# Kernel optimization log

Hardware: AMD Instinct MI355X
Metric: run time of the kernel (lower is better)

## Reference

```python
import jax, jax.numpy as jnp
import numpy as np

B, T, C, H = 2, 2048, 1024, 16
D = C // H
CURV = 1.0  # clamp_curvature(1.0) -> 1.0
EPS = 1e-5


def layer_norm(x, w, b):
    mu = jnp.mean(x, axis=-1, keepdims=True)
    var = jnp.var(x, axis=-1, keepdims=True)
    return (x - mu) * jax.lax.rsqrt(var + EPS) * w + b


def mobius_addition(x, y, c):
    xn2 = jnp.sum(x * x, axis=-1, keepdims=True)
    yn2 = jnp.sum(y * y, axis=-1, keepdims=True)
    ip = jnp.sum(x * y, axis=-1, keepdims=True)
    num = (1 + 2 * c * ip + c * yn2) * x + (1 - c * xn2) * y
    den = 1 + 2 * c * ip + (c ** 2) * xn2 * yn2
    return num / den


def scaling_factor(x, c):
    xn2 = jnp.sum(x * x, axis=-1, keepdims=True)
    return 2.0 / (1.0 + c * xn2)


def expmap(x, v, c):
    lam = scaling_factor(x, c)
    vn = jnp.linalg.norm(v, axis=-1, keepdims=True)
    second = (1.0 / c ** 0.5) * jnp.tanh(jnp.sqrt(c * lam * vn ** 2 / 2.0)) * v / vn
    return mobius_addition(x, second, c)


def logmap(x, u, c):
    lam = scaling_factor(x, c)
    m = mobius_addition(-x, u, c)
    mn = jnp.linalg.norm(m, axis=-1, keepdims=True)
    cf = 2.0 / (lam * c ** 0.5)
    arg = jnp.clip(jnp.sqrt(c * mn), -0.999, 0.999)
    return cf * jnp.arctanh(arg) * m / mn


def calc_reference_point(x):
    # shift-right by one token, zero at position 0
    return jnp.pad(x[:, :-1, :], ((0, 0), (1, 0), (0, 0)))


def causal_attention(q, k, v):
    # q,k,v: [B,H,T,D]
    scores = jnp.einsum('bhqd,bhkd->bhqk', q, k) / np.sqrt(D).astype(np.float32)
    mask = jnp.tril(jnp.ones((T, T), dtype=bool))
    scores = jnp.where(mask, scores, -jnp.inf)
    att = jax.nn.softmax(scores, axis=-1)
    return jnp.einsum('bhqk,bhkd->bhqd', att, v)


def setup_inputs() -> dict:
    key = jax.random.key(0)
    ks = jax.random.split(key, 6)
    s = 0.02
    return {
        'x': jax.random.normal(ks[0], (B, T, C), jnp.float32),
        'ln1_w': jnp.ones((C,), jnp.float32),
        'ln1_b': jnp.zeros((C,), jnp.float32),
        'W_attn': jax.random.normal(ks[1], (C, 3 * C), jnp.float32) * s,
        'b_attn': jnp.zeros((3 * C,), jnp.float32),
        'W_aproj': jax.random.normal(ks[2], (C, C), jnp.float32) * s,
        'b_aproj': jnp.zeros((C,), jnp.float32),
        'ln2_w': jnp.ones((C,), jnp.float32),
        'ln2_b': jnp.zeros((C,), jnp.float32),
        'W_fc': jax.random.normal(ks[3], (C, 4 * C), jnp.float32) * s,
        'b_fc': jnp.zeros((4 * C,), jnp.float32),
        'W_mproj': jax.random.normal(ks[4], (4 * C, C), jnp.float32) * s,
        'b_mproj': jnp.zeros((C,), jnp.float32),
    }


def reference(x, ln1_w, ln1_b, W_attn, b_attn, W_aproj, b_aproj,
              ln2_w, ln2_b, W_fc, b_fc, W_mproj, b_mproj):
    c = CURV
    # --- attention branch ---
    xn = layer_norm(x, ln1_w, ln1_b)
    ref = calc_reference_point(xn)
    xt = logmap(ref, xn, c)
    qkv = xt @ W_attn + b_attn
    q, k, v = jnp.split(qkv, 3, axis=-1)
    q = q.reshape(B, T, H, D).transpose(0, 2, 1, 3)
    k = k.reshape(B, T, H, D).transpose(0, 2, 1, 3)
    v = v.reshape(B, T, H, D).transpose(0, 2, 1, 3)
    y = causal_attention(q, k, v)
    y = y.transpose(0, 2, 1, 3).reshape(B, T, C)
    y = expmap(ref, y, c)  # map_back_after_attention=True
    y = y @ W_aproj + b_aproj
    x = x + y
    # --- MLP branch (no expmap since map_back_after_attention) ---
    h = layer_norm(x, ln2_w, ln2_b)
    h = jax.nn.gelu(h @ W_fc + b_fc, approximate=False)
    h = h @ W_mproj + b_mproj
    return x + h
```

## Files before the change

kernel.cpp:

```cpp
#include <hip/hip_runtime.h>
#include <hip/hip_bf16.h>
#include <math.h>

#define BDIM 2
#define TSEQ 2048
#define CDIM 1024
#define HNUM 16
#define NROW (BDIM*TSEQ)
#define AST 88

typedef __attribute__((ext_vector_type(8))) short bf16x8_t;
typedef __attribute__((ext_vector_type(4))) float f32x4_t;

__device__ inline float bf2f(__hip_bfloat16 h) { return __bfloat162float(h); }

__device__ inline void unpack8(uint4 u, float* f) {
  unsigned v[4] = {u.x, u.y, u.z, u.w};
  #pragma unroll
  for (int i = 0; i < 4; ++i) {
    union { unsigned u2; float f2; } a, b;
    a.u2 = v[i] << 16;
    b.u2 = v[i] & 0xffff0000u;
    f[2*i]   = a.f2;
    f[2*i+1] = b.f2;
  }
}

__device__ inline void gload16(const void* g, void* l) {
  __builtin_amdgcn_global_load_lds(
      (const __attribute__((address_space(1))) void*)g,
      (__attribute__((address_space(3))) void*)l, 16, 0, 0);
}

template<int N> __device__ inline void waitcnt_vm() {
  asm volatile("s_waitcnt vmcnt(%0)" :: "i"(N) : "memory");
}

__global__ __launch_bounds__(256) void zero32_kernel(float* p, int n) {
  int i = blockIdx.x * 256 + threadIdx.x;
  if (i < n) p[i] = 0.f;
}

__global__ __launch_bounds__(256) void convT_kernel(const float* __restrict__ src,
    __hip_bfloat16* __restrict__ dst, int K, int N)
{
  __shared__ float tile[32][33];
  const int k0 = blockIdx.x * 32, n0 = blockIdx.y * 32;
  const int tr  = threadIdx.x >> 3;
  const int tc4 = (threadIdx.x & 7) * 4;
  float4 v = *(const float4*)(src + (size_t)(k0 + tr) * N + n0 + tc4);
  tile[tr][tc4+0] = v.x; tile[tr][tc4+1] = v.y;
  tile[tr][tc4+2] = v.z; tile[tr][tc4+3] = v.w;
  __syncthreads();
  union { ushort4 u; __hip_bfloat16 h[4]; } o;
  #pragma unroll
  for (int j = 0; j < 4; ++j) o.h[j] = __float2bfloat16(tile[tc4+j][tr]);
  *(ushort4*)(dst + (size_t)(n0 + tr) * K + k0 + tc4) = o.u;
}

__device__ inline void blk_reduce3(float& a, float& b, float& c, float* red) {
  const int lane = threadIdx.x & 63, wv = threadIdx.x >> 6;
  #pragma unroll
  for (int off = 32; off; off >>= 1) {
    a += __shfl_xor(a, off); b += __shfl_xor(b, off); c += __shfl_xor(c, off);
  }
  if (lane == 0) { red[wv] = a; red[4+wv] = b; red[8+wv] = c; }
  __syncthreads();
  a = red[0]+red[1]+red[2]+red[3];
  b = red[4]+red[5]+red[6]+red[7];
  c = red[8]+red[9]+red[10]+red[11];
}

__global__ __launch_bounds__(256) void ln_kernel(const float* __restrict__ x,
    const float* __restrict__ w, const float* __restrict__ b,
    __hip_bfloat16* __restrict__ out)
{
  const int row = blockIdx.x;
  const size_t base = (size_t)row * CDIM;
  const int lane = threadIdx.x & 63, wv = threadIdx.x >> 6;
  float v[4]; float s = 0.f, s2 = 0.f;
  #pragma unroll
  for (int k = 0; k < 4; ++k) {
    int d = threadIdx.x + k*256;
    float xe = x[base + d];
    v[k] = xe; s += xe; s2 += xe*xe;
  }
  __shared__ float red[8];
  #pragma unroll
  for (int off = 32; off; off >>= 1) { s += __shfl_xor(s, off); s2 += __shfl_xor(s2, off); }
  if (lane == 0) { red[wv] = s; red[4+wv] = s2; }
  __syncthreads();
  s  = red[0]+red[1]+red[2]+red[3];
  s2 = red[4]+red[5]+red[6]+red[7];
  float mu = s * (1.0f/CDIM);
  float var = s2 * (1.0f/CDIM) - mu*mu;
  float rstd = rsqrtf(fmaxf(var, 0.f) + 1e-5f);
  #pragma unroll
  for (int k = 0; k < 4; ++k) {
    int d = threadIdx.x + k*256;
    out[base + d] = __float2bfloat16((v[k]-mu)*rstd*w[d] + b[d]);
  }
}

__global__ __launch_bounds__(256) void scalmix1_kernel(const __hip_bfloat16* __restrict__ xn,
                                                       __hip_bfloat16* __restrict__ xt)
{
  const int row = blockIdx.x;
  const bool has = (row & (TSEQ-1)) != 0;
  const __hip_bfloat16* u  = xn + (size_t)row * CDIM;
  const __hip_bfloat16* xp = xn + (size_t)(has ? row-1 : row) * CDIM;
  float ue[4], xe[4];
  float sxx = 0.f, suu = 0.f, sxu = 0.f;
  #pragma unroll
  for (int k = 0; k < 4; ++k) {
    int d = threadIdx.x + k*256;
    ue[k] = bf2f(u[d]);
    xe[k] = has ? bf2f(xp[d]) : 0.f;
    sxx += xe[k]*xe[k]; suu += ue[k]*ue[k]; sxu += xe[k]*ue[k];
  }
  __shared__ float red[12];
  blk_reduce3(sxx, suu, sxu, red);
  float den = 1.f - 2.f*sxu + sxx*suu;
  float inv = 1.f / fmaxf(den, 1e-30f);
  float cb = 1.f - sxx;
  float ca = 1.f - 2.f*sxu + suu;
  float mm = inv*inv*(cb*cb*suu - 2.f*ca*cb*sxu + ca*ca*sxx);
  float mn = sqrtf(fmaxf(mm, 0.f));
  float arg = fminf(sqrtf(mn), 0.999f);
  float fac = (1.f + sxx) * atanhf(arg) / fmaxf(mn, 1e-30f);
  float P = fac*cb*inv;
  float Q = has ? -fac*ca*inv : 0.f;
  #pragma unroll
  for (int k = 0; k < 4; ++k) {
    int d = threadIdx.x + k*256;
    xt[(size_t)row*CDIM + d] = __float2bfloat16(P*ue[k] + Q*xe[k]);
  }
}

__global__ __launch_bounds__(256) void scalmix2_kernel(const __hip_bfloat16* __restrict__ xn,
                                                       const __hip_bfloat16* __restrict__ y,
                                                       __hip_bfloat16* __restrict__ e)
{
  const int row = blockIdx.x;
  const bool has = (row & (TSEQ-1)) != 0;
  const __hip_bfloat16* xp = xn + (size_t)(has ? row-1 : row) * CDIM;
  const __hip_bfloat16* vr = y + (size_t)row * CDIM;
  float ve[4], xe[4];
  float sxx = 0.f, svv = 0.f, sxv = 0.f;
  #pragma unroll
  for (int k = 0; k < 4; ++k) {
    int d = threadIdx.x + k*256;
    ve[k] = bf2f(vr[d]);
    xe[k] = has ? bf2f(xp[d]) : 0.f;
    sxx += xe[k]*xe[k]; svv += ve[k]*ve[k]; sxv += xe[k]*ve[k];
  }
  __shared__ float red[12];
  blk_reduce3(sxx, svv, sxv, red);
  float lam = 2.f / (1.f + sxx);
  float vn  = sqrtf(fmaxf(svv, 1e-30f));
  float th  = tanhf(vn * sqrtf(0.5f*lam));
  float s   = th / vn;
  float yn2 = th*th;
  float ip  = s * sxv;
  float den = 1.f + 2.f*ip + sxx*yn2;
  float inv = 1.f / fmaxf(den, 1e-30f);
  float S = (1.f - sxx)*s*inv;
  float R = has ? (1.f + 2.f*ip + yn2)*inv : 0.f;
  #pragma unroll
  for (int k = 0; k < 4; ++k) {
    int d = threadIdx.x + k*256;
    e[(size_t)row*CDIM + d] = __float2bfloat16(S*ve[k] + R*xe[k]);
  }
}

template<int BM, int BN, int MODE>
__global__ __launch_bounds__(256) void gemmT_kernel(
    const __hip_bfloat16* __restrict__ A, int lda,
    const __hip_bfloat16* __restrict__ Bt, int ldb,
    const float* __restrict__ bias,
    const float* __restrict__ res,
    void* __restrict__ outp,
    int N, int K)
{
  __shared__ __align__(16) __hip_bfloat16 As[3][BM*32];
  __shared__ __align__(16) __hip_bfloat16 Bs[3][BN*32];
  const int bm = blockIdx.x, bn = blockIdx.y;
  const int tid = threadIdx.x, lane = tid & 63, wv = tid >> 6;
  constexpr int FM = BM/32, FN = BN/32;
  const int wm = (wv >> 1) * (BM/2), wn = (wv & 1) * (BN/2);
  f32x4_t acc[FM][FN];
  #pragma unroll
  for (int m = 0; m < FM; ++m)
    #pragma unroll
    for (int n = 0; n < FN; ++n) acc[m][n] = (f32x4_t){0.f,0.f,0.f,0.f};

  const int fr = lane & 15, quad = lane >> 4, q8 = quad * 8;
  const int srow = lane >> 2, scol = (lane & 3) * 8;
  constexpr int SA = BM/16, SB = BN/16;
  constexpr int L = SA/4 + SB/4;
  const __hip_bfloat16* Ag = A  + (size_t)(bm*BM + srow)*lda + scol;
  const __hip_bfloat16* Bg = Bt + (size_t)(bn*BN + srow)*ldb + scol;

  const int nk = K/32;

  #pragma unroll
  for (int i = 0; i < SA/4; ++i) {
    int s = wv*(SA/4) + i;
    gload16(Ag + (size_t)(s*16)*lda, &As[0][s*512]);
  }
  #pragma unroll
  for (int i = 0; i < SB/4; ++i) {
    int s = wv*(SB/4) + i;
    gload16(Bg + (size_t)(s*16)*ldb, &Bs[0][s*512]);
  }
  #pragma unroll
  for (int i = 0; i < SA/4; ++i) {
    int s = wv*(SA/4) + i;
    gload16(Ag + (size_t)(s*16)*lda + 32, &As[1][s*512]);
  }
  #pragma unroll
  for (int i = 0; i < SB/4; ++i) {
    int s = wv*(SB/4) + i;
    gload16(Bg + (size_t)(s*16)*ldb + 32, &Bs[1][s*512]);
  }

  int b0 = 0, b1 = 1, b2 = 2;
  for (int t = 0; t < nk; ++t) {
    if (t + 1 < nk) waitcnt_vm<L>(); else waitcnt_vm<0>();
    __builtin_amdgcn_s_barrier();
    __builtin_amdgcn_sched_barrier(0);
    if (t + 2 < nk) {
      const int k0 = (t+2)*32;
      #pragma unroll
      for (int i = 0; i < SA/4; ++i) {
        int s = wv*(SA/4) + i;
        gload16(Ag + (size_t)(s*16)*lda + k0, &As[b2][s*512]);
      }
      #pragma unroll
      for (int i = 0; i < SB/4; ++i) {
        int s = wv*(SB/4) + i;
        gload16(Bg + (size_t)(s*16)*ldb + k0, &Bs[b2][s*512]);
      }
    }
    bf16x8_t af[FM], bfr[FN];
    #pragma unroll
    for (int m = 0; m < FM; ++m) af[m]  = *(const bf16x8_t*)&As[b0][(wm + m*16 + fr)*32 + q8];
    #pragma unroll
    for (int n = 0; n < FN; ++n) bfr[n] = *(const bf16x8_t*)&Bs[b0][(wn + n*16 + fr)*32 + q8];
    __builtin_amdgcn_s_setprio(1);
    #pragma unroll
    for (int m = 0; m < FM; ++m)
      #pragma unroll
      for (int n = 0; n < FN; ++n)
        acc[m][n] = __builtin_amdgcn_mfma_f32_16x16x32_bf16(af[m], bfr[n], acc[m][n], 0, 0, 0);
    __builtin_amdgcn_s_setprio(0);
    int tmp = b0; b0 = b1; b1 = b2; b2 = tmp;
  }

  #pragma unroll
  for (int m = 0; m < FM; ++m)
  #pragma unroll
  for (int n = 0; n < FN; ++n)
  #pragma unroll
  for (int r = 0; r < 4; ++r) {
    int row = bm*BM + wm + m*16 + quad*4 + r;
    int col = bn*BN + wn + n*16 + fr;
    size_t idx = (size_t)row * N + col;
    float v = acc[m][n][r];
    if (MODE == 0) {
      v += bias[col];
      ((__hip_bfloat16*)outp)[idx] = __float2bfloat16(v);
    } else if (MODE == 1) {
      v += bias[col] + res[idx];
      ((float*)outp)[idx] = v;
    } else if (MODE == 2) {
      v += bias[col];
      v = 0.5f * v * (1.0f + erff(v * 0.70710678118654752f));
      ((__hip_bfloat16*)outp)[idx] = __float2bfloat16(v);
    } else {
      v += res[idx];
      ((float*)outp)[idx] = v;
    }
  }
}

__device__ inline __hip_bfloat16* slot_ptr(__hip_bfloat16* p0, __hip_bfloat16* p1, int s) {
  return (s < 2048) ? p0 + (size_t)s*4096 : p1 + (size_t)(s-2048)*4096;
}

__global__ __launch_bounds__(256) void attn_kernel(const __hip_bfloat16* __restrict__ qkv,
                                                   __hip_bfloat16* __restrict__ y,
                                                   __hip_bfloat16* __restrict__ pO0,
                                                   __hip_bfloat16* __restrict__ pO1,
                                                   float2* __restrict__ ml)
{
  const int wid = blockIdx.x;
  int qt, ci;
  if (wid < 32)      { qt = 31 - (wid >> 2); ci = wid & 3; }
  else if (wid < 56) { int w = wid - 32; qt = 23 - w/3; ci = w - (23 - qt)*3; }
  else if (wid < 72) { int w = wid - 56; qt = 15 - (w >> 1); ci = w & 1; }
  else               { qt = 79 - wid; ci = 0; }
  const int tb = ci * 8;
  const int te = min(tb + 8, qt + 1);
  const bool direct = (qt < 8);

  const int pair = blockIdx.y;
  const int b  = pair >> 4;
  const int h  = pair & 15;
  const int tid = threadIdx.x;
  const int lane = tid & 63;
  const int wv = tid >> 6;
  const int t0 = qt * 64;

  __shared__ __align__(16) __hip_bfloat16 Ks[64*AST];
  __shared__ __align__(16) __hip_bfloat16 Vt[64*AST];
  __shared__ __align__(16) __hip_bfloat16 Ps[4][16*AST];

  const int colq = lane & 15, quad = lane >> 4;
  const int q8 = quad * 8;

  const __hip_bfloat16* qp = qkv + ((size_t)(b*TSEQ + t0 + wv*16 + colq))*(3*CDIM) + h*64;
  const bf16x8_t qa0 = *(const bf16x8_t*)(qp + q8);
  const bf16x8_t qa1 = *(const bf16x8_t*)(qp + 32 + q8);

  f32x4_t oacc[4];
  #pragma unroll
  for (int tn = 0; tn < 4; ++tn) oacc[tn] = (f32x4_t){0.f,0.f,0.f,0.f};
  float mr[4] = {-1e30f,-1e30f,-1e30f,-1e30f};
  float lr[4] = {0.f,0.f,0.f,0.f};

  const int jr = tid >> 2;
  const int sg = (tid & 3) * 16;
  const size_t kvbase = ((size_t)(b*TSEQ))*(3*CDIM) + h*64;

  uint4 ck0, ck1, cv0, cv1;
  {
    const __hip_bfloat16* kp = qkv + kvbase + (size_t)(tb*64 + jr)*(3*CDIM) + CDIM + sg;
    ck0 = *(const uint4*)(kp);
    ck1 = *(const uint4*)(kp + 8);
    cv0 = *(const uint4*)(kp + CDIM);
    cv1 = *(const uint4*)(kp + CDIM + 8);
  }
  uint4 nk0 = ck0, nk1 = ck1, nv0 = cv0, nv1 = cv1;

  for (int t = tb; t < te; ++t) {
    __syncthreads();
    {
      *(uint4*)(&Ks[jr*AST + sg])     = ck0;
      *(uint4*)(&Ks[jr*AST + sg + 8]) = ck1;
      union { uint4 u; __hip_bfloat16 hh[8]; } a0, a1;
      a0.u = cv0; a1.u = cv1;
      #pragma unroll
      for (int e = 0; e < 8; ++e) Vt[(sg + e)*AST + jr]     = a0.hh[e];
      #pragma unroll
      for (int e = 0; e < 8; ++e) Vt[(sg + 8 + e)*AST + jr] = a1.hh[e];
    }
    if (t + 1 < te) {
      const __hip_bfloat16* kp = qkv + kvbase + (size_t)((t+1)*64 + jr)*(3*CDIM) + CDIM + sg;
      nk0 = *(const uint4*)(kp);
      nk1 = *(const uint4*)(kp + 8);
      nv0 = *(const uint4*)(kp + CDIM);
      nv1 = *(const uint4*)(kp + CDIM + 8);
    }
    __syncthreads();

    f32x4_t sacc[4];
    __builtin_amdgcn_s_setprio(1);
    #pragma unroll
    for (int tn = 0; tn < 4; ++tn) {
      sacc[tn] = (f32x4_t){0.f,0.f,0.f,0.f};
      bf16x8_t bk0 = *(const bf16x8_t*)(&Ks[(tn*16 + colq)*AST + q8]);
      sacc[tn] = __builtin_amdgcn_mfma_f32_16x16x32_bf16(qa0, bk0, sacc[tn], 0, 0, 0);
      bf16x8_t bk1 = *(const bf16x8_t*)(&Ks[(tn*16 + colq)*AST + 32 + q8]);
      sacc[tn] = __builtin_amdgcn_mfma_f32_16x16x32_bf16(qa1, bk1, sacc[tn], 0, 0, 0);
    }
    __builtin_amdgcn_s_setprio(0);

    float sc[4][4];
    #pragma unroll
    for (int tn = 0; tn < 4; ++tn)
    #pragma unroll
    for (int r = 0; r < 4; ++r) sc[tn][r] = sacc[tn][r] * 0.125f;
    if (t == qt) {
      #pragma unroll
      for (int tn = 0; tn < 4; ++tn)
      #pragma unroll
      for (int r = 0; r < 4; ++r) {
        int key = t*64 + tn*16 + colq;
        int row = t0 + wv*16 + quad*4 + r;
        if (key > row) sc[tn][r] = -1e30f;
      }
    }

    float mx[4];
    #pragma unroll
    for (int r = 0; r < 4; ++r) {
      mx[r] = fmaxf(fmaxf(sc[0][r], sc[1][r]), fmaxf(sc[2][r], sc[3][r]));
      #pragma unroll
      for (int off = 8; off; off >>= 1) mx[r] = fmaxf(mx[r], __shfl_xor(mx[r], off));
    }
    bool grow = (mx[0] > mr[0] + 8.f) || (mx[1] > mr[1] + 8.f) ||
                (mx[2] > mr[2] + 8.f) || (mx[3] > mr[3] + 8.f);
    if (__any(grow)) {
      #pragma unroll
      for (int r = 0; r < 4; ++r) {
        float mn = fmaxf(mr[r], mx[r]);
        float al = __expf(mr[r] - mn);
        mr[r] = mn;
        lr[r] *= al;
        #pragma unroll
        for (int tn = 0; tn < 4; ++tn) oacc[tn][r] *= al;
      }
    }
    float psum[4] = {0.f,0.f,0.f,0.f};
    #pragma unroll
    for (int tn = 0; tn < 4; ++tn)
    #pragma unroll
    for (int r = 0; r < 4; ++r) {
      float p = __expf(sc[tn][r] - mr[r]);
      psum[r] += p;
      Ps[wv][(quad*4 + r)*AST + tn*16 + colq] = __float2bfloat16(p);
    }
    #pragma unroll
    for (int r = 0; r < 4; ++r) {
      #pragma unroll
      for (int off = 8; off; off >>= 1) psum[r] += __shfl_xor(psum[r], off);
      lr[r] += psum[r];
    }

    bf16x8_t pa0 = *(const bf16x8_t*)(&Ps[wv][colq*AST + q8]);
    bf16x8_t pa1 = *(const bf16x8_t*)(&Ps[wv][colq*AST + 32 + q8]);
    __builtin_amdgcn_s_setprio(1);
    #pragma unroll
    for (int tn = 0; tn < 4; ++tn) {
      bf16x8_t vb0 = *(const bf16x8_t*)(&Vt[(tn*16 + colq)*AST + q8]);
      oacc[tn] = __builtin_amdgcn_mfma_f32_16x16x32_bf16(pa0, vb0, oacc[tn], 0, 0, 0);
      bf16x8_t vb1 = *(const bf16x8_t*)(&Vt[(tn*16 + colq)*AST + 32 + q8]);
      oacc[tn] = __builtin_amdgcn_mfma_f32_16x16x32_bf16(pa1, vb1, oacc[tn], 0, 0, 0);
    }
    __builtin_amdgcn_s_setprio(0);

    ck0 = nk0; ck1 = nk1; cv0 = nv0; cv1 = nv1;
  }

  if (direct) {
    __hip_bfloat16* yp = y + ((size_t)(b*TSEQ + t0 + wv*16))*CDIM + h*64;
    #pragma unroll
    for (int tn = 0; tn < 4; ++tn)
    #pragma unroll
    for (int r = 0; r < 4; ++r) {
      yp[(size_t)(quad*4 + r)*CDIM + tn*16 + colq] = __float2bfloat16(oacc[tn][r] / lr[r]);
    }
  } else {
    int off = (qt >= 24) ? 40 + (qt-24)*4 : (qt >= 16) ? 16 + (qt-16)*3 : (qt-8)*2;
    int s = pair*72 + off + ci;
    __hip_bfloat16* op = slot_ptr(pO0, pO1, s);
    #pragma unroll
    for (int tn = 0; tn < 4; ++tn)
    #pragma unroll
    for (int r = 0; r < 4; ++r) {
      op[wv*1024 + tn*256 + r*64 + lane] = __float2bfloat16(oacc[tn][r]);
    }
    if (colq == 0) {
      #pragma unroll
      for (int r = 0; r < 4; ++r)
        ml[(size_t)s*64 + wv*16 + quad*4 + r] = make_float2(mr[r], lr[r]);
    }
  }
}

__global__ __launch_bounds__(256) void combine_kernel(__hip_bfloat16* __restrict__ pO0,
                                                      __hip_bfloat16* __restrict__ pO1,
                                                      const float2* __restrict__ ml,
                                                      __hip_bfloat16* __restrict__ y)
{
  const int qt = 8 + blockIdx.x;
  const int pair = blockIdx.y;
  const int b = pair >> 4, h = pair & 15;
  const int nch = (qt >= 24) ? 4 : (qt >= 16) ? 3 : 2;
  const int off = (qt >= 24) ? 40 + (qt-24)*4 : (qt >= 16) ? 16 + (qt-16)*3 : (qt-8)*2;
  const int s0 = pair*72 + off;
  const int tid = threadIdx.x;
  const int q = tid >> 2;
  const int dseg = (tid & 3) * 16;

  float mi[4], li[4];
  float M = -1e30f;
  #pragma unroll
  for (int i = 0; i < 4; ++i) {
    if (i < nch) {
      float2 t = ml[(size_t)(s0+i)*64 + q];
      mi[i] = t.x; li[i] = t.y;
      M = fmaxf(M, t.x);
    }
  }
  float w[4]; float denom = 0.f;
  #pragma unroll
  for (int i = 0; i < 4; ++i) {
    if (i < nch) { w[i] = __expf(mi[i] - M); denom += li[i]*w[i]; }
  }
  const int base = (q >> 4)*1024 + (dseg >> 4)*256 + (q & 3)*64 + ((q >> 2) & 3)*16;
  float acc[16];
  #pragma unroll
  for (int j = 0; j < 16; ++j) acc[j] = 0.f;
  #pragma unroll
  for (int i = 0; i < 4; ++i) {
    if (i < nch) {
      const __hip_bfloat16* op = slot_ptr(pO0, pO1, s0+i) + base;
      uint4 u0 = *(const uint4*)(op);
      uint4 u1 = *(const uint4*)(op + 8);
      float f[16];
      unpack8(u0, f); unpack8(u1, f+8);
      #pragma unroll
      for (int j = 0; j < 16; ++j) acc[j] += w[i]*f[j];
    }
  }
  float inv = 1.f / denom;
  union { uint4 u[2]; __hip_bfloat16 hh[16]; } o;
  #pragma unroll
  for (int j = 0; j < 16; ++j) o.hh[j] = __float2bfloat16(acc[j]*inv);
  __hip_bfloat16* yp = y + ((size_t)(b*TSEQ + qt*64 + q))*CDIM + h*64 + dseg;
  *(uint4*)(yp) = o.u[0];
  *(uint4*)(yp + 8) = o.u[1];
}

extern "C" void kernel_launch(void* const* d_in, const int* in_sizes, int n_in,
                              void* d_out, int out_size, void* d_ws, size_t ws_size,
                              hipStream_t stream)
{
  float* out = (float*)d_out;
  __hip_bfloat16* ybuf = (__hip_bfloat16*)d_out;
  float* x2d = (float*)d_out;
  char* ws = (char*)d_ws;
  const size_t KB = 1024, MB = 1024*1024;

  if (ws_size < 49*MB) {
    zero32_kernel<<<(out_size + 255)/256, 256, 0, stream>>>(out, out_size);
    return;
  }

  const float* x      = (const float*)d_in[0];
  const float* ln1w   = (const float*)d_in[1];
  const float* ln1b   = (const float*)d_in[2];
  const float* Wattn  = (const float*)d_in[3];
  const float* battn  = (const float*)d_in[4];
  const float* Waproj = (const float*)d_in[5];
  const float* baproj = (const float*)d_in[6];
  const float* ln2w   = (const float*)d_in[7];
  const float* ln2b   = (const float*)d_in[8];
  const float* Wfc    = (const float*)d_in[9];
  const float* bfc    = (const float*)d_in[10];
  const float* Wmproj = (const float*)d_in[11];
  const float* bmproj = (const float*)d_in[12];

  __hip_bfloat16* xn   = (__hip_bfloat16*)(ws + 64*KB);
  char* big            = ws + 64*KB + 8*MB;
  __hip_bfloat16* qkv  = (__hip_bfloat16*)big;
  __hip_bfloat16* gbuf = (__hip_bfloat16*)big;
  __hip_bfloat16* ebuf = (__hip_bfloat16*)(big + 16*MB);
  __hip_bfloat16* hbuf = xn;
  char* creg           = ws + 64*KB + 32*MB;
  __hip_bfloat16* cWattnT  = (__hip_bfloat16*)creg;
  __hip_bfloat16* xt       = (__hip_bfloat16*)(creg + 8*MB);
  __hip_bfloat16* cWaprojT = (__hip_bfloat16*)creg;
  __hip_bfloat16* cWfcT    = (__hip_bfloat16*)creg;
  __hip_bfloat16* cWmT     = (__hip_bfloat16*)(creg + 8*MB);
  __hip_bfloat16* pO0      = (__hip_bfloat16*)creg;
  __hip_bfloat16* pO1      = (__hip_bfloat16*)((char*)d_out + 8*MB);
  float2* mlbuf            = (float2*)((char*)d_out + 10*MB);

  convT_kernel<<<dim3(32, 96), 256, 0, stream>>>(Wattn,  cWattnT,  1024, 3072);

  ln_kernel<<<NROW, 256, 0, stream>>>(x, ln1w, ln1b, xn);
  scalmix1_kernel<<<NROW, 256, 0, stream>>>(xn, xt);
  gemmT_kernel<128,128,0><<<dim3(32, 24), 256, 0, stream>>>(
      xt, 1024, cWattnT, 1024, battn, nullptr, qkv, 3072, 1024);
  attn_kernel<<<dim3(80, BDIM*HNUM), 256, 0, stream>>>(qkv, ybuf, pO0, pO1, mlbuf);
  combine_kernel<<<dim3(24, BDIM*HNUM), 256, 0, stream>>>(pO0, pO1, mlbuf, ybuf);
  convT_kernel<<<dim3(32, 32), 256, 0, stream>>>(Waproj, cWaprojT, 1024, 1024);
  scalmix2_kernel<<<NROW, 256, 0, stream>>>(xn, ybuf, ebuf);
  gemmT_kernel<64,64,1><<<dim3(64, 16), 256, 0, stream>>>(
      ebuf, 1024, cWaprojT, 1024, baproj, x, x2d, 1024, 1024);
  convT_kernel<<<dim3(32, 128), 256, 0, stream>>>(Wfc,    cWfcT, 1024, 4096);
  convT_kernel<<<dim3(128, 32), 256, 0, stream>>>(Wmproj, cWmT,  4096, 1024);
  ln_kernel<<<NROW, 256, 0, stream>>>(x2d, ln2w, ln2b, hbuf);
  for (int c = 0; c < 2; ++c) {
    gemmT_kernel<64,128,2><<<dim3(64, 16), 256, 0, stream>>>(
        hbuf, 1024, cWfcT + (size_t)c*2048*1024, 1024, bfc + 2048*c, nullptr, gbuf,
        2048, 1024);
    const __hip_bfloat16* Bc = cWmT + 2048*c;
    if (c == 0) {
      gemmT_kernel<64,64,1><<<dim3(64, 16), 256, 0, stream>>>(
          gbuf, 2048, Bc, 4096, bmproj, x2d, x2d, 1024, 2048);
    } else {
      gemmT_kernel<64,64,7><<<dim3(64, 16), 256, 0, stream>>>(
          gbuf, 2048, Bc, 4096, nullptr, x2d, out, 1024, 2048);
    }
  }
}
```

Before: 440.4 us.

## Fuse split-KV combine into scalmix2, merge weight conversions, lazy softmax rescale

The separate combine kernel is removed. scalmix2 now merges the partial attention outputs directly, using the stored max/sum pairs, before the expmap mixing, so the merged y never goes through global memory. The two FC weight transpose-conversions become one launch. The attention softmax now computes exponentials against the running max first and only recomputes with a new max if the partial sum overflows a threshold, which skips the max reduction in the common case. The LDS row stride is reduced from 88 to 72. The fused combine does scalar, uncoalesced per-element loads and recomputes weights per element, and the lazy rescale computes exponentials twice whenever it triggers.

```diff
diff --git a/kernel.cpp b/kernel.cpp
--- a/kernel.cpp
+++ b/kernel.cpp
@@ -7,7 +7,7 @@
 #define CDIM 1024
 #define HNUM 16
 #define NROW (BDIM*TSEQ)
-#define AST 88
+#define AST 72
 
 typedef __attribute__((ext_vector_type(8))) short bf16x8_t;
 typedef __attribute__((ext_vector_type(4))) float f32x4_t;
@@ -41,11 +41,11 @@
   if (i < n) p[i] = 0.f;
 }
 
-__global__ __launch_bounds__(256) void convT_kernel(const float* __restrict__ src,
-    __hip_bfloat16* __restrict__ dst, int K, int N)
+__device__ inline void convT_body(const float* __restrict__ src,
+    __hip_bfloat16* __restrict__ dst, int K, int N, int bx, int by)
 {
   __shared__ float tile[32][33];
-  const int k0 = blockIdx.x * 32, n0 = blockIdx.y * 32;
+  const int k0 = bx * 32, n0 = by * 32;
   const int tr  = threadIdx.x >> 3;
   const int tc4 = (threadIdx.x & 7) * 4;
   float4 v = *(const float4*)(src + (size_t)(k0 + tr) * N + n0 + tc4);
@@ -56,6 +56,25 @@
   #pragma unroll
   for (int j = 0; j < 4; ++j) o.h[j] = __float2bfloat16(tile[tc4+j][tr]);
   *(ushort4*)(dst + (size_t)(n0 + tr) * K + k0 + tc4) = o.u;
+}
+
+__global__ __launch_bounds__(256) void convT_kernel(const float* __restrict__ src,
+    __hip_bfloat16* __restrict__ dst, int K, int N)
+{
+  convT_body(src, dst, K, N, blockIdx.x, blockIdx.y);
+}
+
+__global__ __launch_bounds__(256) void convT2_kernel(const float* __restrict__ s1,
+    __hip_bfloat16* __restrict__ d1, const float* __restrict__ s2,
+    __hip_bfloat16* __restrict__ d2)
+{
+  int g = blockIdx.x;
+  if (g < 4096) {
+    convT_body(s1, d1, 1024, 4096, g & 31, g >> 5);
+  } else {
+    g -= 4096;
+    convT_body(s2, d2, 4096, 1024, g & 127, g >> 7);
+  }
 }
 
 __device__ inline void blk_reduce3(float& a, float& b, float& c, float* red) {
@@ -137,20 +156,61 @@
   }
 }
 
+__device__ inline const __hip_bfloat16* slot_ptrc(const __hip_bfloat16* p0,
+                                                  const __hip_bfloat16* p1, int s) {
+  return (s < 2048) ? p0 + (size_t)s*4096 : p1 + (size_t)(s-2048)*4096;
+}
+__device__ inline __hip_bfloat16* slot_ptr(__hip_bfloat16* p0, __hip_bfloat16* p1, int s) {
+  return (s < 2048) ? p0 + (size_t)s*4096 : p1 + (size_t)(s-2048)*4096;
+}
+
 __global__ __launch_bounds__(256) void scalmix2_kernel(const __hip_bfloat16* __restrict__ xn,
-                                                       const __hip_bfloat16* __restrict__ y,
-                                                       __hip_bfloat16* __restrict__ e)
+    const __hip_bfloat16* __restrict__ y,
+    const __hip_bfloat16* __restrict__ pO0, const __hip_bfloat16* __restrict__ pO1,
+    const float2* __restrict__ ml,
+    __hip_bfloat16* __restrict__ e)
 {
   const int row = blockIdx.x;
-  const bool has = (row & (TSEQ-1)) != 0;
+  const int b = row >> 11, t = row & 2047;
+  const int qt = t >> 6, q = t & 63;
+  const bool has = (t != 0);
   const __hip_bfloat16* xp = xn + (size_t)(has ? row-1 : row) * CDIM;
-  const __hip_bfloat16* vr = y + (size_t)row * CDIM;
   float ve[4], xe[4];
+
+  if (qt < 8) {
+    const __hip_bfloat16* vr = y + (size_t)row * CDIM;
+    #pragma unroll
+    for (int k = 0; k < 4; ++k) ve[k] = bf2f(vr[threadIdx.x + k*256]);
+  } else {
+    const int nch = (qt >= 24) ? 4 : (qt >= 16) ? 3 : 2;
+    const int off = (qt >= 24) ? 40 + (qt-24)*4 : (qt >= 16) ? 16 + (qt-16)*3 : (qt-8)*2;
+    #pragma unroll
+    for (int k = 0; k < 4; ++k) {
+      int d = threadIdx.x + k*256;
+      int h = d >> 6, dd = d & 63;
+      int s0 = (b*16 + h)*72 + off;
+      float mi[4], li[4], M = -1e30f;
+      #pragma unroll
+      for (int i = 0; i < 4; ++i) if (i < nch) {
+        float2 tt = ml[(size_t)(s0+i)*64 + q];
+        mi[i] = tt.x; li[i] = tt.y; M = fmaxf(M, tt.x);
+      }
+      int base = (q>>4)*1024 + (dd>>4)*256 + (q&3)*64 + ((q>>2)&3)*16 + (dd&15);
+      float denom = 0.f, acc = 0.f;
+      #pragma unroll
+      for (int i = 0; i < 4; ++i) if (i < nch) {
+        float w = __expf(mi[i] - M);
+        denom += li[i]*w;
+        acc += w * bf2f(slot_ptrc(pO0, pO1, s0+i)[base]);
+      }
+      ve[k] = acc / denom;
+    }
+  }
+
   float sxx = 0.f, svv = 0.f, sxv = 0.f;
   #pragma unroll
   for (int k = 0; k < 4; ++k) {
     int d = threadIdx.x + k*256;
-    ve[k] = bf2f(vr[d]);
     xe[k] = has ? bf2f(xp[d]) : 0.f;
     sxx += xe[k]*xe[k]; svv += ve[k]*ve[k]; sxv += xe[k]*ve[k];
   }
@@ -284,10 +344,6 @@
   }
 }
 
-__device__ inline __hip_bfloat16* slot_ptr(__hip_bfloat16* p0, __hip_bfloat16* p1, int s) {
-  return (s < 2048) ? p0 + (size_t)s*4096 : p1 + (size_t)(s-2048)*4096;
-}
-
 __global__ __launch_bounds__(256) void attn_kernel(const __hip_bfloat16* __restrict__ qkv,
                                                    __hip_bfloat16* __restrict__ y,
                                                    __hip_bfloat16* __restrict__ pO0,
@@ -392,16 +448,30 @@
       }
     }
 
-    float mx[4];
+    float psum[4] = {0.f,0.f,0.f,0.f};
+    #pragma unroll
+    for (int tn = 0; tn < 4; ++tn)
     #pragma unroll
     for (int r = 0; r < 4; ++r) {
-      mx[r] = fmaxf(fmaxf(sc[0][r], sc[1][r]), fmaxf(sc[2][r], sc[3][r]));
-      #pragma unroll
-      for (int off = 8; off; off >>= 1) mx[r] = fmaxf(mx[r], __shfl_xor(mx[r], off));
-    }
-    bool grow = (mx[0] > mr[0] + 8.f) || (mx[1] > mr[1] + 8.f) ||
-                (mx[2] > mr[2] + 8.f) || (mx[3] > mr[3] + 8.f);
-    if (__any(grow)) {
+      float p = __expf(sc[tn][r] - mr[r]);
+      psum[r] += p;
+      Ps[wv][(quad*4 + r)*AST + tn*16 + colq] = __float2bfloat16(p);
+    }
+    #pragma unroll
+    for (int r = 0; r < 4; ++r) {
+      #pragma unroll
+      for (int off = 8; off; off >>= 1) psum[r] += __shfl_xor(psum[r], off);
+    }
+    bool trig = !(psum[0] <= 1e5f) || !(psum[1] <= 1e5f) ||
+                !(psum[2] <= 1e5f) || !(psum[3] <= 1e5f);
+    if (__any(trig)) {
+      float mx[4];
+      #pragma unroll
+      for (int r = 0; r < 4; ++r) {
+        mx[r] = fmaxf(fmaxf(sc[0][r], sc[1][r]), fmaxf(sc[2][r], sc[3][r]));
+        #pragma unroll
+        for (int off = 8; off; off >>= 1) mx[r] = fmaxf(mx[r], __shfl_xor(mx[r], off));
+      }
       #pragma unroll
       for (int r = 0; r < 4; ++r) {
         float mn = fmaxf(mr[r], mx[r]);
@@ -410,23 +480,24 @@
         lr[r] *= al;
         #pragma unroll
         for (int tn = 0; tn < 4; ++tn) oacc[tn][r] *= al;
-      }
-    }
-    float psum[4] = {0.f,0.f,0.f,0.f};
-    #pragma unroll
-    for (int tn = 0; tn < 4; ++tn)
-    #pragma unroll
-    for (int r = 0; r < 4; ++r) {
-      float p = __expf(sc[tn][r] - mr[r]);
-      psum[r] += p;
-      Ps[wv][(quad*4 + r)*AST + tn*16 + colq] = __float2bfloat16(p);
-    }
-    #pragma unroll
-    for (int r = 0; r < 4; ++r) {
-      #pragma unroll
-      for (int off = 8; off; off >>= 1) psum[r] += __shfl_xor(psum[r], off);
-      lr[r] += psum[r];
-    }
+        psum[r] = 0.f;
+      }
+      #pragma unroll
+      for (int tn = 0; tn < 4; ++tn)
+      #pragma unroll
+      for (int r = 0; r < 4; ++r) {
+        float p = __expf(sc[tn][r] - mr[r]);
+        psum[r] += p;
+        Ps[wv][(quad*4 + r)*AST + tn*16 + colq] = __float2bfloat16(p);
+      }
+      #pragma unroll
+      for (int r = 0; r < 4; ++r) {
+        #pragma unroll
+        for (int off = 8; off; off >>= 1) psum[r] += __shfl_xor(psum[r], off);
+      }
+    }
+    #pragma unroll
+    for (int r = 0; r < 4; ++r) lr[r] += psum[r];
 
     bf16x8_t pa0 = *(const bf16x8_t*)(&Ps[wv][colq*AST + q8]);
     bf16x8_t pa1 = *(const bf16x8_t*)(&Ps[wv][colq*AST + 32 + q8]);
@@ -467,61 +538,6 @@
         ml[(size_t)s*64 + wv*16 + quad*4 + r] = make_float2(mr[r], lr[r]);
     }
   }
-}
-
-__global__ __launch_bounds__(256) void combine_kernel(__hip_bfloat16* __restrict__ pO0,
-                                                      __hip_bfloat16* __restrict__ pO1,
-                                                      const float2* __restrict__ ml,
-                                                      __hip_bfloat16* __restrict__ y)
-{
-  const int qt = 8 + blockIdx.x;
-  const int pair = blockIdx.y;
-  const int b = pair >> 4, h = pair & 15;
-  const int nch = (qt >= 24) ? 4 : (qt >= 16) ? 3 : 2;
-  const int off = (qt >= 24) ? 40 + (qt-24)*4 : (qt >= 16) ? 16 + (qt-16)*3 : (qt-8)*2;
-  const int s0 = pair*72 + off;
-  const int tid = threadIdx.x;
-  const int q = tid >> 2;
-  const int dseg = (tid & 3) * 16;
-
-  float mi[4], li[4];
-  float M = -1e30f;
-  #pragma unroll
-  for (int i = 0; i < 4; ++i) {
-    if (i < nch) {
-      float2 t = ml[(size_t)(s0+i)*64 + q];
-      mi[i] = t.x; li[i] = t.y;
-      M = fmaxf(M, t.x);
-    }
-  }
-  float w[4]; float denom = 0.f;
-  #pragma unroll
-  for (int i = 0; i < 4; ++i) {
-    if (i < nch) { w[i] = __expf(mi[i] - M); denom += li[i]*w[i]; }
-  }
-  const int base = (q >> 4)*1024 + (dseg >> 4)*256 + (q & 3)*64 + ((q >> 2) & 3)*16;
-  float acc[16];
-  #pragma unroll
-  for (int j = 0; j < 16; ++j) acc[j] = 0.f;
-  #pragma unroll
-  for (int i = 0; i < 4; ++i) {
-    if (i < nch) {
-      const __hip_bfloat16* op = slot_ptr(pO0, pO1, s0+i) + base;
-      uint4 u0 = *(const uint4*)(op);
-      uint4 u1 = *(const uint4*)(op + 8);
-      float f[16];
-      unpack8(u0, f); unpack8(u1, f+8);
-      #pragma unroll
-      for (int j = 0; j < 16; ++j) acc[j] += w[i]*f[j];
-    }
-  }
-  float inv = 1.f / denom;
-  union { uint4 u[2]; __hip_bfloat16 hh[16]; } o;
-  #pragma unroll
-  for (int j = 0; j < 16; ++j) o.hh[j] = __float2bfloat16(acc[j]*inv);
-  __hip_bfloat16* yp = y + ((size_t)(b*TSEQ + qt*64 + q))*CDIM + h*64 + dseg;
-  *(uint4*)(yp) = o.u[0];
-  *(uint4*)(yp + 8) = o.u[1];
 }
 
 extern "C" void kernel_launch(void* const* d_in, const int* in_sizes, int n_in,
@@ -576,13 +592,11 @@
   gemmT_kernel<128,128,0><<<dim3(32, 24), 256, 0, stream>>>(
       xt, 1024, cWattnT, 1024, battn, nullptr, qkv, 3072, 1024);
   attn_kernel<<<dim3(80, BDIM*HNUM), 256, 0, stream>>>(qkv, ybuf, pO0, pO1, mlbuf);
-  combine_kernel<<<dim3(24, BDIM*HNUM), 256, 0, stream>>>(pO0, pO1, mlbuf, ybuf);
+  scalmix2_kernel<<<NROW, 256, 0, stream>>>(xn, ybuf, pO0, pO1, mlbuf, ebuf);
   convT_kernel<<<dim3(32, 32), 256, 0, stream>>>(Waproj, cWaprojT, 1024, 1024);
-  scalmix2_kernel<<<NROW, 256, 0, stream>>>(xn, ybuf, ebuf);
   gemmT_kernel<64,64,1><<<dim3(64, 16), 256, 0, stream>>>(
       ebuf, 1024, cWaprojT, 1024, baproj, x, x2d, 1024, 1024);
-  convT_kernel<<<dim3(32, 128), 256, 0, stream>>>(Wfc,    cWfcT, 1024, 4096);
-  convT_kernel<<<dim3(128, 32), 256, 0, stream>>>(Wmproj, cWmT,  4096, 1024);
+  convT2_kernel<<<8192, 256, 0, stream>>>(Wfc, cWfcT, Wmproj, cWmT);
   ln_kernel<<<NROW, 256, 0, stream>>>(x2d, ln2w, ln2b, hbuf);
   for (int c = 0; c < 2; ++c) {
     gemmT_kernel<64,128,2><<<dim3(64, 16), 256, 0, stream>>>(
```

Result: slower. 455.7 us (+3.5%).
